# Kernel optimization log

Hardware: AMD Instinct MI355X
Metric: run time of the kernel (lower is better)

## Reference

```python
import jax, jax.numpy as jnp
import numpy as np

N_USERS, N_ITEMS, EMB, NNZ, B = 60000, 40000, 64, 2560000, 4096
N_LAYERS = 3


def setup_inputs() -> dict:
    key = jax.random.key(0)
    ks = jax.random.split(key, 16)
    N = N_USERS + N_ITEMS
    return {
        "user_emb": jax.random.normal(ks[0], (N_USERS, EMB), jnp.float32) * 0.1,
        "item_emb": jax.random.normal(ks[1], (N_ITEMS, EMB), jnp.float32) * 0.1,
        "W_gc": jax.random.normal(ks[2], (N_LAYERS, EMB, EMB), jnp.float32) * (1.0 / np.sqrt(EMB)),
        "b_gc": jax.random.normal(ks[3], (N_LAYERS, 1, EMB), jnp.float32) * 0.01,
        "W_bi": jax.random.normal(ks[4], (N_LAYERS, EMB, EMB), jnp.float32) * (1.0 / np.sqrt(EMB)),
        "b_bi": jax.random.normal(ks[5], (N_LAYERS, 1, EMB), jnp.float32) * 0.01,
        "adj_vals": jax.random.uniform(ks[6], (NNZ,), jnp.float32) * (1.0 / 25.6),
        "adj_rows": jax.random.randint(ks[7], (NNZ,), 0, N, jnp.int32),
        "adj_cols": jax.random.randint(ks[8], (NNZ,), 0, N, jnp.int32),
        "user_sizes": jax.random.randint(ks[9], (N_USERS,), 1, EMB + 1, jnp.int32),
        "item_sizes": jax.random.randint(ks[10], (N_ITEMS,), 1, EMB + 1, jnp.int32),
        "users": jax.random.randint(ks[11], (B,), 0, N_USERS, jnp.int32),
        "pos_items": jax.random.randint(ks[12], (B,), 0, N_ITEMS, jnp.int32),
        "neg_items": jax.random.randint(ks[13], (B,), 0, N_ITEMS, jnp.int32),
    }


def _computer(user_emb, item_emb, W_gc, b_gc, W_bi, b_bi,
              adj_vals, adj_rows, adj_cols, user_sizes, item_sizes):
    n_user = user_emb.shape[0]
    N = n_user + item_emb.shape[0]
    d = user_emb.shape[1]
    ar = jnp.arange(d, dtype=jnp.int32)
    user_mask = (ar[None, :] < user_sizes[:, None]).astype(user_emb.dtype)
    item_mask = (ar[None, :] < item_sizes[:, None]).astype(item_emb.dtype)
    ego = jnp.concatenate([user_emb * user_mask, item_emb * item_mask], axis=0)  # [N, d]
    all_embeddings = [ego]
    for k in range(W_gc.shape[0]):
        # sparse A_hat @ ego  (COO SpMM via gather + segment_sum)
        side = jax.ops.segment_sum(adj_vals[:, None] * ego[adj_cols],
                                   adj_rows, num_segments=N)  # [N, d]
        sum_emb = side @ W_gc[k] + b_gc[k]
        bi_emb = (ego * side) @ W_bi[k] + b_bi[k]
        ego = jax.nn.leaky_relu(sum_emb + bi_emb, negative_slope=0.2)
        # mess_dropout = 0 (eval); L2-normalize rows (F.normalize, eps=1e-12)
        norm = jnp.maximum(jnp.linalg.norm(ego, axis=1, keepdims=True), 1e-12)
        all_embeddings.append(ego / norm)
    all_emb = jnp.concatenate(all_embeddings, axis=1)  # [N, d*(L+1)]
    return all_emb[:n_user], all_emb[n_user:]


def reference(user_emb, item_emb, W_gc, b_gc, W_bi, b_bi,
              adj_vals, adj_rows, adj_cols, user_sizes, item_sizes,
              users, pos_items, neg_items):
    u_g, i_g = _computer(user_emb, item_emb, W_gc, b_gc, W_bi, b_bi,
                         adj_vals, adj_rows, adj_cols, user_sizes, item_sizes)
    return (u_g[users], i_g[pos_items], i_g[neg_items])
```

## Files before the change

kernel.cpp:

```cpp
#include <hip/hip_runtime.h>

#define EMB 64
constexpr int N_LAYERS = 3;
constexpr int OUT_D = EMB * (N_LAYERS + 1);
constexpr int SUBR = 64;
constexpr int RSHIFT = 6;
constexpr int MAXBUK = 2048;
constexpr int PAD = 16;
constexpr int CHUNK = 4096;
constexpr int EPT = CHUNK / 256;

__device__ __forceinline__ float readlane_f(float v, int l) {
  return __int_as_float(__builtin_amdgcn_readlane(__float_as_int(v), l));
}
__device__ __forceinline__ int readlane_i(int v, int l) {
  return __builtin_amdgcn_readlane(v, l);
}

__global__ void init_ego_kernel(const float* __restrict__ ue, const float* __restrict__ ie,
                                const int* __restrict__ usz, const int* __restrict__ isz,
                                float* __restrict__ ego, float* __restrict__ all_emb,
                                int n_users, int n_total) {
  int idx = blockIdx.x * blockDim.x + threadIdx.x;
  if (idx >= n_total * EMB) return;
  int r = idx >> 6, d = idx & 63;
  float v; int sz;
  if (r < n_users) {
    v = ue[idx];
    sz = usz[r];
  } else {
    int ri = r - n_users;
    v = ie[ri * EMB + d];
    sz = isz[ri];
  }
  v = (d < sz) ? v : 0.0f;
  ego[idx] = v;
  all_emb[(size_t)r * OUT_D + d] = v;
}

__global__ __launch_bounds__(256) void bucket_hist_kernel(const int* __restrict__ rows,
                                                          int* __restrict__ bcnt_pad,
                                                          int nnz, int nbuk) {
  __shared__ int h[MAXBUK];
  for (int i = threadIdx.x; i < nbuk; i += 256) h[i] = 0;
  __syncthreads();
  int i = blockIdx.x * blockDim.x + threadIdx.x;
  int stride = gridDim.x * blockDim.x;
  for (; i < nnz; i += stride) atomicAdd(&h[rows[i] >> RSHIFT], 1);
  __syncthreads();
  for (int b = threadIdx.x; b < nbuk; b += 256)
    if (h[b]) atomicAdd(&bcnt_pad[b * PAD], h[b]);
}

__global__ __launch_bounds__(512) void bucket_scan_kernel(const int* __restrict__ bcnt_pad,
                                                          int* __restrict__ bbase,
                                                          int* __restrict__ bcursor_pad,
                                                          int nbuk) {
  __shared__ int vals[MAXBUK];
  __shared__ int part[512];
  int t = threadIdx.x;
  for (int i = t; i < nbuk; i += 512) vals[i] = bcnt_pad[i * PAD];
  __syncthreads();
  int per = (nbuk + 511) / 512;
  int s0 = t * per;
  int lsum = 0;
  for (int i = 0; i < per; ++i) {
    int idx = s0 + i;
    if (idx < nbuk) lsum += vals[idx];
  }
  part[t] = lsum;
  __syncthreads();
  if (t == 0) {
    int acc = 0;
    for (int i = 0; i < 512; ++i) {
      int x = part[i];
      part[i] = acc;
      acc += x;
    }
  }
  __syncthreads();
  int run = part[t];
  for (int i = 0; i < per; ++i) {
    int idx = s0 + i;
    if (idx < nbuk) {
      bbase[idx] = run;
      bcursor_pad[idx * PAD] = run;
      run += vals[idx];
    }
  }
  if (t == 511) bbase[nbuk] = run;
}

__global__ __launch_bounds__(256) void partition_lds_kernel(
    const float* __restrict__ vals, const int* __restrict__ rows,
    const int* __restrict__ cols, int* __restrict__ bcursor_pad,
    int2* __restrict__ tmp, int nnz, int nbuk) {
  __shared__ int h[MAXBUK];
  __shared__ int cur[MAXBUK];
  for (int i = threadIdx.x; i < nbuk; i += 256) h[i] = 0;
  __syncthreads();

  int base = blockIdx.x * CHUNK;
  int rw[EPT], cl[EPT];
  float vl[EPT];
#pragma unroll
  for (int u = 0; u < EPT; ++u) {
    int ii = base + u * 256 + (int)threadIdx.x;
    bool ok = ii < nnz;
    rw[u] = ok ? rows[ii] : -1;
    cl[u] = ok ? cols[ii] : 0;
    vl[u] = ok ? vals[ii] : 0.0f;
    if (ok) atomicAdd(&h[rw[u] >> RSHIFT], 1);
  }
  __syncthreads();
  for (int b = threadIdx.x; b < nbuk; b += 256) {
    int c = h[b];
    cur[b] = c ? atomicAdd(&bcursor_pad[b * PAD], c) : 0;
  }
  __syncthreads();
#pragma unroll
  for (int u = 0; u < EPT; ++u) {
    if (rw[u] >= 0) {
      int b = rw[u] >> RSHIFT;
      int pos = atomicAdd(&cur[b], 1);
      tmp[pos] = make_int2(__float_as_int(vl[u]),
                           ((rw[u] & (SUBR - 1)) << 17) | cl[u]);
    }
  }
}

__global__ __launch_bounds__(256) void bucket_sort_kernel(
    const int2* __restrict__ tmp, const int* __restrict__ bbase,
    int2* __restrict__ edges, int* __restrict__ row_ptr, int nrows) {
  __shared__ int h[SUBR];
  __shared__ int ex[SUBR + 1];
  int b = blockIdx.x;
  int s = bbase[b], e = bbase[b + 1];
  if (threadIdx.x < SUBR) h[threadIdx.x] = 0;
  __syncthreads();
  for (int i = s + (int)threadIdx.x; i < e; i += 256)
    atomicAdd(&h[((unsigned)tmp[i].y) >> 17], 1);
  __syncthreads();
  if (threadIdx.x == 0) {
    int acc = 0;
    for (int j = 0; j < SUBR; ++j) {
      ex[j] = acc;
      acc += h[j];
    }
    ex[SUBR] = acc;
  }
  __syncthreads();
  int r0 = b << RSHIFT;
  if (threadIdx.x <= SUBR) {
    int j = threadIdx.x;
    int r = r0 + j;
    if ((j < SUBR && r < nrows) || r == nrows) row_ptr[r] = s + ex[j];
  }
  if (threadIdx.x < SUBR) h[threadIdx.x] = ex[threadIdx.x];
  __syncthreads();
  for (int i = s + (int)threadIdx.x; i < e; i += 256) {
    int2 t = tmp[i];
    int rl = ((unsigned)t.y) >> 17;
    int p = atomicAdd(&h[rl], 1);
    edges[s + p] = make_int2(t.x, t.y & 0x1FFFF);
  }
}

__global__ __launch_bounds__(256) void spmm_csr_kernel(
    const int* __restrict__ rp, const int2* __restrict__ edges,
    const float* __restrict__ ego, float* __restrict__ side, int nrows) {
  int lane = threadIdx.x & 63;
  int r = blockIdx.x * (blockDim.x >> 6) + (threadIdx.x >> 6);
  if (r >= nrows) return;
  int start = rp[r], end = rp[r + 1];
  float acc = 0.0f;
  for (int base = start; base < end; base += 64) {
    int m = end - base;
    if (m > 64) m = 64;
    int2 e = (base + lane < end) ? edges[base + lane] : make_int2(0, 0);
    float v_l = __int_as_float(e.x);
    int c_l = e.y;
    int kk = 0;
    for (; kk + 8 <= m; kk += 8) {
      int c[8];
      float v[8], x[8];
#pragma unroll
      for (int u = 0; u < 8; ++u) {
        c[u] = readlane_i(c_l, kk + u);
        v[u] = readlane_f(v_l, kk + u);
      }
#pragma unroll
      for (int u = 0; u < 8; ++u) x[u] = ego[(size_t)c[u] * EMB + lane];
#pragma unroll
      for (int u = 0; u < 8; ++u) acc = fmaf(v[u], x[u], acc);
    }
    for (; kk < m; ++kk) {
      int c = readlane_i(c_l, kk);
      float v = readlane_f(v_l, kk);
      acc = fmaf(v, ego[(size_t)c * EMB + lane], acc);
    }
  }
  side[(size_t)r * EMB + lane] = acc;
}

__global__ __launch_bounds__(256) void layer_fused_kernel(
    const float* __restrict__ side, float* ego,
    const float* __restrict__ Wgc, const float* __restrict__ bgc,
    const float* __restrict__ Wbi, const float* __restrict__ bbi,
    float* __restrict__ all_emb, int nrows, int col_off) {
  int lane = threadIdx.x & 63;
  float wgc[EMB], wbi[EMB];
#pragma unroll
  for (int kk = 0; kk < EMB; ++kk) {
    wgc[kk] = Wgc[kk * EMB + lane];
    wbi[kk] = Wbi[kk * EMB + lane];
  }
  float bg = bgc[lane], bb = bbi[lane];
  int wid = blockIdx.x * (blockDim.x >> 6) + (threadIdx.x >> 6);
  int nw = gridDim.x * (blockDim.x >> 6);
  for (int r = wid; r < nrows; r += nw) {
    float s = side[(size_t)r * EMB + lane];
    float e = ego[(size_t)r * EMB + lane];
    float es = e * s;
    float accg = bg, accb = bb;
#pragma unroll
    for (int kk = 0; kk < EMB; ++kk) {
      accg = fmaf(readlane_f(s, kk), wgc[kk], accg);
      accb = fmaf(readlane_f(es, kk), wbi[kk], accb);
    }
    float o = accg + accb;
    o = (o >= 0.0f) ? o : 0.2f * o;
    ego[(size_t)r * EMB + lane] = o;
    float sq = o * o;
#pragma unroll
    for (int off = 32; off; off >>= 1) sq += __shfl_xor(sq, off, 64);
    float norm = fmaxf(sqrtf(sq), 1e-12f);
    all_emb[(size_t)r * OUT_D + col_off + lane] = o / norm;
  }
}

__global__ void gather_out_kernel(const float* __restrict__ all_emb,
                                  const int* __restrict__ users,
                                  const int* __restrict__ pos,
                                  const int* __restrict__ neg,
                                  float* __restrict__ out, int n_users, int B) {
  int row = blockIdx.x;
  int sec = blockIdx.y;
  int t = threadIdx.x;
  int src;
  if (sec == 0) src = users[row];
  else if (sec == 1) src = n_users + pos[row];
  else src = n_users + neg[row];
  out[((size_t)sec * B + row) * OUT_D + t] = all_emb[(size_t)src * OUT_D + t];
}

extern "C" void kernel_launch(void* const* d_in, const int* in_sizes, int n_in,
                              void* d_out, int out_size, void* d_ws, size_t ws_size,
                              hipStream_t stream) {
  const float* user_emb = (const float*)d_in[0];
  const float* item_emb = (const float*)d_in[1];
  const float* W_gc = (const float*)d_in[2];
  const float* b_gc = (const float*)d_in[3];
  const float* W_bi = (const float*)d_in[4];
  const float* b_bi = (const float*)d_in[5];
  const float* adj_vals = (const float*)d_in[6];
  const int* adj_rows = (const int*)d_in[7];
  const int* adj_cols = (const int*)d_in[8];
  const int* user_sizes = (const int*)d_in[9];
  const int* item_sizes = (const int*)d_in[10];
  const int* users = (const int*)d_in[11];
  const int* pos_items = (const int*)d_in[12];
  const int* neg_items = (const int*)d_in[13];

  const int n_users = in_sizes[9];
  const int n_items = in_sizes[10];
  const int N = n_users + n_items;
  const int nnz = in_sizes[6];
  const int B = in_sizes[11];
  const int nbuk = (N + SUBR - 1) / SUBR;

  float* all_emb = (float*)d_ws;
  float* ego = all_emb + (size_t)N * OUT_D;
  float* side = ego + (size_t)N * EMB;
  int* row_ptr = (int*)(side + (size_t)N * EMB);
  int* bbase = row_ptr + (N + 1);
  int* bcnt_pad = bbase + (nbuk + 1);
  int* bcursor_pad = bcnt_pad + (size_t)nbuk * PAD;
  int2* edges = (int2*)((((uintptr_t)(bcursor_pad + (size_t)nbuk * PAD)) + 7) &
                        ~(uintptr_t)7);
  int2* tmp = (int2*)all_emb;

  hipMemsetAsync(bcnt_pad, 0, (size_t)nbuk * PAD * sizeof(int), stream);
  hipLaunchKernelGGL(bucket_hist_kernel, dim3(512), dim3(256), 0, stream,
                     adj_rows, bcnt_pad, nnz, nbuk);
  hipLaunchKernelGGL(bucket_scan_kernel, dim3(1), dim3(512), 0, stream,
                     bcnt_pad, bbase, bcursor_pad, nbuk);
  {
    int nchunks = (nnz + CHUNK - 1) / CHUNK;
    hipLaunchKernelGGL(partition_lds_kernel, dim3(nchunks), dim3(256), 0,
                       stream, adj_vals, adj_rows, adj_cols, bcursor_pad, tmp,
                       nnz, nbuk);
  }
  hipLaunchKernelGGL(bucket_sort_kernel, dim3(nbuk), dim3(256), 0, stream, tmp,
                     bbase, edges, row_ptr, N);

  {
    int total = N * EMB;
    hipLaunchKernelGGL(init_ego_kernel, dim3((total + 255) / 256), dim3(256), 0,
                       stream, user_emb, item_emb, user_sizes, item_sizes, ego,
                       all_emb, n_users, N);
  }

  for (int k = 0; k < N_LAYERS; ++k) {
    hipLaunchKernelGGL(spmm_csr_kernel, dim3((N + 3) / 4), dim3(256), 0, stream,
                       row_ptr, edges, ego, side, N);
    hipLaunchKernelGGL(layer_fused_kernel, dim3(2048), dim3(256), 0, stream,
                       side, ego, W_gc + k * EMB * EMB, b_gc + k * EMB,
                       W_bi + k * EMB * EMB, b_bi + k * EMB, all_emb, N,
                       (k + 1) * EMB);
  }

  hipLaunchKernelGGL(gather_out_kernel, dim3(B, 3), dim3(256), 0, stream,
                     all_emb, users, pos_items, neg_items, (float*)d_out,
                     n_users, B);
}
```

Measured before the change: 706.3 us.

## Gather bf16 copy of embeddings in SpMM and restructure partition loop

Keeps a bf16 shadow copy of the ego embeddings, written by the init and layer kernels, and has the SpMM gather read that copy instead of the fp32 one, halving gather bytes per edge. Separately, the partition kernel now uses a larger chunk and re-reads rows, cols and vals from global memory in a second pass instead of holding them in registers. The bf16 gather loses precision in the aggregation, and the extra bf16 buffer is placed after the edges in the workspace.

```diff
diff --git a/kernel.cpp b/kernel.cpp
--- a/kernel.cpp
+++ b/kernel.cpp
@@ -7,8 +7,7 @@
 constexpr int RSHIFT = 6;
 constexpr int MAXBUK = 2048;
 constexpr int PAD = 16;
-constexpr int CHUNK = 4096;
-constexpr int EPT = CHUNK / 256;
+constexpr int CHUNK = 8192;
 
 __device__ __forceinline__ float readlane_f(float v, int l) {
   return __int_as_float(__builtin_amdgcn_readlane(__float_as_int(v), l));
@@ -16,11 +15,18 @@
 __device__ __forceinline__ int readlane_i(int v, int l) {
   return __builtin_amdgcn_readlane(v, l);
 }
+__device__ __forceinline__ unsigned short f32_to_bf16(float f) {
+  unsigned x = __float_as_uint(f);
+  return (unsigned short)((x + 0x7FFF + ((x >> 16) & 1)) >> 16);
+}
+__device__ __forceinline__ float bf16_to_f32(unsigned short u) {
+  return __uint_as_float(((unsigned)u) << 16);
+}
 
 __global__ void init_ego_kernel(const float* __restrict__ ue, const float* __restrict__ ie,
                                 const int* __restrict__ usz, const int* __restrict__ isz,
-                                float* __restrict__ ego, float* __restrict__ all_emb,
-                                int n_users, int n_total) {
+                                float* __restrict__ ego, unsigned short* __restrict__ egobf,
+                                float* __restrict__ all_emb, int n_users, int n_total) {
   int idx = blockIdx.x * blockDim.x + threadIdx.x;
   if (idx >= n_total * EMB) return;
   int r = idx >> 6, d = idx & 63;
@@ -35,6 +41,7 @@
   }
   v = (d < sz) ? v : 0.0f;
   ego[idx] = v;
+  egobf[idx] = f32_to_bf16(v);
   all_emb[(size_t)r * OUT_D + d] = v;
 }
 
@@ -99,33 +106,23 @@
   __shared__ int cur[MAXBUK];
   for (int i = threadIdx.x; i < nbuk; i += 256) h[i] = 0;
   __syncthreads();
-
-  int base = blockIdx.x * CHUNK;
-  int rw[EPT], cl[EPT];
-  float vl[EPT];
-#pragma unroll
-  for (int u = 0; u < EPT; ++u) {
-    int ii = base + u * 256 + (int)threadIdx.x;
-    bool ok = ii < nnz;
-    rw[u] = ok ? rows[ii] : -1;
-    cl[u] = ok ? cols[ii] : 0;
-    vl[u] = ok ? vals[ii] : 0.0f;
-    if (ok) atomicAdd(&h[rw[u] >> RSHIFT], 1);
-  }
+  int lo = blockIdx.x * CHUNK;
+  int hi = lo + CHUNK;
+  if (hi > nnz) hi = nnz;
+  for (int ii = lo + (int)threadIdx.x; ii < hi; ii += 256)
+    atomicAdd(&h[rows[ii] >> RSHIFT], 1);
   __syncthreads();
   for (int b = threadIdx.x; b < nbuk; b += 256) {
     int c = h[b];
     cur[b] = c ? atomicAdd(&bcursor_pad[b * PAD], c) : 0;
   }
   __syncthreads();
-#pragma unroll
-  for (int u = 0; u < EPT; ++u) {
-    if (rw[u] >= 0) {
-      int b = rw[u] >> RSHIFT;
-      int pos = atomicAdd(&cur[b], 1);
-      tmp[pos] = make_int2(__float_as_int(vl[u]),
-                           ((rw[u] & (SUBR - 1)) << 17) | cl[u]);
-    }
+  for (int ii = lo + (int)threadIdx.x; ii < hi; ii += 256) {
+    int r = rows[ii];
+    int b = r >> RSHIFT;
+    int pos = atomicAdd(&cur[b], 1);
+    tmp[pos] = make_int2(__float_as_int(vals[ii]),
+                         ((r & (SUBR - 1)) << 17) | cols[ii]);
   }
 }
 
@@ -168,7 +165,8 @@
 
 __global__ __launch_bounds__(256) void spmm_csr_kernel(
     const int* __restrict__ rp, const int2* __restrict__ edges,
-    const float* __restrict__ ego, float* __restrict__ side, int nrows) {
+    const unsigned short* __restrict__ egobf, float* __restrict__ side,
+    int nrows) {
   int lane = threadIdx.x & 63;
   int r = blockIdx.x * (blockDim.x >> 6) + (threadIdx.x >> 6);
   if (r >= nrows) return;
@@ -190,21 +188,22 @@
         v[u] = readlane_f(v_l, kk + u);
       }
 #pragma unroll
-      for (int u = 0; u < 8; ++u) x[u] = ego[(size_t)c[u] * EMB + lane];
+      for (int u = 0; u < 8; ++u)
+        x[u] = bf16_to_f32(egobf[(size_t)c[u] * EMB + lane]);
 #pragma unroll
       for (int u = 0; u < 8; ++u) acc = fmaf(v[u], x[u], acc);
     }
     for (; kk < m; ++kk) {
       int c = readlane_i(c_l, kk);
       float v = readlane_f(v_l, kk);
-      acc = fmaf(v, ego[(size_t)c * EMB + lane], acc);
+      acc = fmaf(v, bf16_to_f32(egobf[(size_t)c * EMB + lane]), acc);
     }
   }
   side[(size_t)r * EMB + lane] = acc;
 }
 
 __global__ __launch_bounds__(256) void layer_fused_kernel(
-    const float* __restrict__ side, float* ego,
+    const float* __restrict__ side, float* ego, unsigned short* __restrict__ egobf,
     const float* __restrict__ Wgc, const float* __restrict__ bgc,
     const float* __restrict__ Wbi, const float* __restrict__ bbi,
     float* __restrict__ all_emb, int nrows, int col_off) {
@@ -231,6 +230,7 @@
     float o = accg + accb;
     o = (o >= 0.0f) ? o : 0.2f * o;
     ego[(size_t)r * EMB + lane] = o;
+    egobf[(size_t)r * EMB + lane] = f32_to_bf16(o);
     float sq = o * o;
 #pragma unroll
     for (int off = 32; off; off >>= 1) sq += __shfl_xor(sq, off, 64);
@@ -288,6 +288,7 @@
   int* bcursor_pad = bcnt_pad + (size_t)nbuk * PAD;
   int2* edges = (int2*)((((uintptr_t)(bcursor_pad + (size_t)nbuk * PAD)) + 7) &
                         ~(uintptr_t)7);
+  unsigned short* egobf = (unsigned short*)(edges + nnz);
   int2* tmp = (int2*)all_emb;
 
   hipMemsetAsync(bcnt_pad, 0, (size_t)nbuk * PAD * sizeof(int), stream);
@@ -308,14 +309,14 @@
     int total = N * EMB;
     hipLaunchKernelGGL(init_ego_kernel, dim3((total + 255) / 256), dim3(256), 0,
                        stream, user_emb, item_emb, user_sizes, item_sizes, ego,
-                       all_emb, n_users, N);
+                       egobf, all_emb, n_users, N);
   }
 
   for (int k = 0; k < N_LAYERS; ++k) {
     hipLaunchKernelGGL(spmm_csr_kernel, dim3((N + 3) / 4), dim3(256), 0, stream,
-                       row_ptr, edges, ego, side, N);
+                       row_ptr, edges, egobf, side, N);
     hipLaunchKernelGGL(layer_fused_kernel, dim3(2048), dim3(256), 0, stream,
-                       side, ego, W_gc + k * EMB * EMB, b_gc + k * EMB,
+                       side, ego, egobf, W_gc + k * EMB * EMB, b_gc + k * EMB,
                        W_bi + k * EMB * EMB, b_bi + k * EMB, all_emb, N,
                        (k + 1) * EMB);
   }
```

After: 696.0 us. No clear change (-1.5%).

## Gather bf16 copy of ego in SpMM and split layer FMA chains

Applied to the files above, without the earlier changes.

Keeps a bf16 shadow copy of the ego embeddings, written by the init and layer kernels, and has the SpMM gather read 2-byte values instead of fp32. This halves the bytes moved by the random row gathers, which dominate the SpMM. The layer kernel also splits its dot-product accumulation into four independent chains for more instruction-level parallelism, and its grid size is doubled. The cost is bf16 rounding error in the neighbour aggregation and an extra workspace buffer placed after the edges array.

```diff
diff --git a/kernel.cpp b/kernel.cpp
--- a/kernel.cpp
+++ b/kernel.cpp
@@ -16,11 +16,18 @@
 __device__ __forceinline__ int readlane_i(int v, int l) {
   return __builtin_amdgcn_readlane(v, l);
 }
+__device__ __forceinline__ unsigned short f32_to_bf16(float f) {
+  unsigned x = __float_as_uint(f);
+  return (unsigned short)((x + 0x7FFF + ((x >> 16) & 1)) >> 16);
+}
+__device__ __forceinline__ float bf16_to_f32(unsigned short u) {
+  return __uint_as_float(((unsigned)u) << 16);
+}
 
 __global__ void init_ego_kernel(const float* __restrict__ ue, const float* __restrict__ ie,
                                 const int* __restrict__ usz, const int* __restrict__ isz,
-                                float* __restrict__ ego, float* __restrict__ all_emb,
-                                int n_users, int n_total) {
+                                float* __restrict__ ego, unsigned short* __restrict__ egobf,
+                                float* __restrict__ all_emb, int n_users, int n_total) {
   int idx = blockIdx.x * blockDim.x + threadIdx.x;
   if (idx >= n_total * EMB) return;
   int r = idx >> 6, d = idx & 63;
@@ -35,6 +42,7 @@
   }
   v = (d < sz) ? v : 0.0f;
   ego[idx] = v;
+  egobf[idx] = f32_to_bf16(v);
   all_emb[(size_t)r * OUT_D + d] = v;
 }
 
@@ -168,7 +176,8 @@
 
 __global__ __launch_bounds__(256) void spmm_csr_kernel(
     const int* __restrict__ rp, const int2* __restrict__ edges,
-    const float* __restrict__ ego, float* __restrict__ side, int nrows) {
+    const unsigned short* __restrict__ egobf, float* __restrict__ side,
+    int nrows) {
   int lane = threadIdx.x & 63;
   int r = blockIdx.x * (blockDim.x >> 6) + (threadIdx.x >> 6);
   if (r >= nrows) return;
@@ -190,21 +199,22 @@
         v[u] = readlane_f(v_l, kk + u);
       }
 #pragma unroll
-      for (int u = 0; u < 8; ++u) x[u] = ego[(size_t)c[u] * EMB + lane];
+      for (int u = 0; u < 8; ++u)
+        x[u] = bf16_to_f32(egobf[(size_t)c[u] * EMB + lane]);
 #pragma unroll
       for (int u = 0; u < 8; ++u) acc = fmaf(v[u], x[u], acc);
     }
     for (; kk < m; ++kk) {
       int c = readlane_i(c_l, kk);
       float v = readlane_f(v_l, kk);
-      acc = fmaf(v, ego[(size_t)c * EMB + lane], acc);
+      acc = fmaf(v, bf16_to_f32(egobf[(size_t)c * EMB + lane]), acc);
     }
   }
   side[(size_t)r * EMB + lane] = acc;
 }
 
 __global__ __launch_bounds__(256) void layer_fused_kernel(
-    const float* __restrict__ side, float* ego,
+    const float* __restrict__ side, float* ego, unsigned short* __restrict__ egobf,
     const float* __restrict__ Wgc, const float* __restrict__ bgc,
     const float* __restrict__ Wbi, const float* __restrict__ bbi,
     float* __restrict__ all_emb, int nrows, int col_off) {
@@ -222,15 +232,23 @@
     float s = side[(size_t)r * EMB + lane];
     float e = ego[(size_t)r * EMB + lane];
     float es = e * s;
-    float accg = bg, accb = bb;
-#pragma unroll
-    for (int kk = 0; kk < EMB; ++kk) {
-      accg = fmaf(readlane_f(s, kk), wgc[kk], accg);
-      accb = fmaf(readlane_f(es, kk), wbi[kk], accb);
-    }
-    float o = accg + accb;
+    float g0 = 0.f, g1 = 0.f, g2 = 0.f, g3 = 0.f;
+    float h0 = 0.f, h1 = 0.f, h2 = 0.f, h3 = 0.f;
+#pragma unroll
+    for (int kk = 0; kk < EMB; kk += 4) {
+      g0 = fmaf(readlane_f(s, kk + 0), wgc[kk + 0], g0);
+      g1 = fmaf(readlane_f(s, kk + 1), wgc[kk + 1], g1);
+      g2 = fmaf(readlane_f(s, kk + 2), wgc[kk + 2], g2);
+      g3 = fmaf(readlane_f(s, kk + 3), wgc[kk + 3], g3);
+      h0 = fmaf(readlane_f(es, kk + 0), wbi[kk + 0], h0);
+      h1 = fmaf(readlane_f(es, kk + 1), wbi[kk + 1], h1);
+      h2 = fmaf(readlane_f(es, kk + 2), wbi[kk + 2], h2);
+      h3 = fmaf(readlane_f(es, kk + 3), wbi[kk + 3], h3);
+    }
+    float o = (((g0 + g1) + (g2 + g3)) + bg) + (((h0 + h1) + (h2 + h3)) + bb);
     o = (o >= 0.0f) ? o : 0.2f * o;
     ego[(size_t)r * EMB + lane] = o;
+    egobf[(size_t)r * EMB + lane] = f32_to_bf16(o);
     float sq = o * o;
 #pragma unroll
     for (int off = 32; off; off >>= 1) sq += __shfl_xor(sq, off, 64);
@@ -288,6 +306,7 @@
   int* bcursor_pad = bcnt_pad + (size_t)nbuk * PAD;
   int2* edges = (int2*)((((uintptr_t)(bcursor_pad + (size_t)nbuk * PAD)) + 7) &
                         ~(uintptr_t)7);
+  unsigned short* egobf = (unsigned short*)(edges + nnz);
   int2* tmp = (int2*)all_emb;
 
   hipMemsetAsync(bcnt_pad, 0, (size_t)nbuk * PAD * sizeof(int), stream);
@@ -308,14 +327,14 @@
     int total = N * EMB;
     hipLaunchKernelGGL(init_ego_kernel, dim3((total + 255) / 256), dim3(256), 0,
                        stream, user_emb, item_emb, user_sizes, item_sizes, ego,
-                       all_emb, n_users, N);
+                       egobf, all_emb, n_users, N);
   }
 
   for (int k = 0; k < N_LAYERS; ++k) {
     hipLaunchKernelGGL(spmm_csr_kernel, dim3((N + 3) / 4), dim3(256), 0, stream,
-                       row_ptr, edges, ego, side, N);
-    hipLaunchKernelGGL(layer_fused_kernel, dim3(2048), dim3(256), 0, stream,
-                       side, ego, W_gc + k * EMB * EMB, b_gc + k * EMB,
+                       row_ptr, edges, egobf, side, N);
+    hipLaunchKernelGGL(layer_fused_kernel, dim3(4096), dim3(256), 0, stream,
+                       side, ego, egobf, W_gc + k * EMB * EMB, b_gc + k * EMB,
                        W_bi + k * EMB * EMB, b_bi + k * EMB, all_emb, N,
                        (k + 1) * EMB);
   }
```

Result: faster. 681.4 us (-3.5%).
